# Kernel optimization log

Hardware: AMD Instinct MI355X
Metric: run time of the kernel (lower is better)

## Reference

```python
import jax, jax.numpy as jnp
import numpy as np

N = 50000      # nodes
K = 32         # fixed neighbor count per node
D_IN, D_HID, D_OUT = 512, 128, 64


def setup_inputs() -> dict:
    key = jax.random.key(0)
    k1, k2, k3, k4 = jax.random.split(key, 4)
    feat = jax.random.normal(k1, (N, D_IN), dtype=jnp.float32)
    W1 = jax.random.normal(k2, (D_IN, D_HID), dtype=jnp.float32) * (1.0 / np.sqrt(D_IN))
    b1 = jnp.zeros((D_HID,), dtype=jnp.float32)
    W2 = jax.random.normal(k3, (D_HID, D_OUT), dtype=jnp.float32) * (1.0 / np.sqrt(D_HID))
    b2 = jnp.zeros((D_OUT,), dtype=jnp.float32)
    neighbors = jax.random.randint(k4, (N, K), 0, N, dtype=jnp.int64)
    return {"feat": feat, "W1": W1, "b1": b1, "W2": W2, "b2": b2,
            "neighbors": neighbors}


def _median_conv(x, W, b, neighbors):
    # linear transform, then per-node median over neighbor messages
    h = x @ W + b                      # [N, D]
    nb = h[neighbors]                  # [N, K, D]  gather (irregular access)
    # torch.median returns the lower middle element for even K
    med = jnp.sort(nb, axis=1)[:, (K - 1) // 2]   # [N, D]
    return med


def reference(feat, W1, b1, W2, b2, neighbors):
    # MedianGCN forward (eval mode: dropout is identity), norm='none'
    h = jax.nn.relu(_median_conv(feat, W1, b1, neighbors))
    out = _median_conv(h, W2, b2, neighbors)
    return out
```

## Files before the change

### kernel.cpp

```cpp
#include <hip/hip_runtime.h>
#include <cstddef>

#define NN   50000
#define KNB  32

typedef _Float16 h2    __attribute__((ext_vector_type(2)));
typedef _Float16 half8 __attribute__((ext_vector_type(8)));
typedef float    f4    __attribute__((ext_vector_type(4)));
typedef float    f8    __attribute__((ext_vector_type(8)));

__global__ __launch_bounds__(256) void prep(const float* __restrict__ W1,
                                            const float* __restrict__ W2,
                                            _Float16* __restrict__ w1t,
                                            _Float16* __restrict__ w2t) {
  const int id = blockIdx.x * 256 + threadIdx.x;
  if (id < 128 * 512) {
    const int n = id >> 9, k = id & 511;
    w1t[id] = (_Float16)W1[k * 128 + n];
  } else {
    const int id2 = id - 128 * 512;
    if (id2 < 64 * 128) {
      const int n = id2 >> 7, k = id2 & 127;
      w2t[id2] = (_Float16)W2[k * 64 + n];
    }
  }
}

__global__ __launch_bounds__(256) void gemm1_mfma(
    const float* __restrict__ A, const _Float16* __restrict__ Bt,
    const float* __restrict__ bias, _Float16* __restrict__ C, int M) {
  constexpr int K = 512;
  const int wave = threadIdx.x >> 6;
  const int lane = threadIdx.x & 63;
  const int m0   = blockIdx.x * 64 + wave * 16;
  const int mr   = lane & 15;
  const int kg   = lane >> 4;

  int arow = m0 + mr;
  if (arow >= M) arow = M - 1;
  const float*    ap = A  + (size_t)arow * K + kg * 8;
  const _Float16* bp = Bt + (size_t)mr   * K + kg * 8;

  f4 acc[8] = {};

  #pragma unroll 2
  for (int k0 = 0; k0 < K; k0 += 32) {
    const f4 a0 = *(const f4*)ap;
    const f4 a1 = *(const f4*)(ap + 4);
    const f8 av = {a0[0], a0[1], a0[2], a0[3], a1[0], a1[1], a1[2], a1[3]};
    const half8 af = __builtin_convertvector(av, half8);
    #pragma unroll
    for (int nt = 0; nt < 8; ++nt) {
      const half8 bf = *(const half8*)(bp + (size_t)nt * 16 * K);
      acc[nt] = __builtin_amdgcn_mfma_f32_16x16x32_f16(af, bf, acc[nt], 0, 0, 0);
    }
    ap += 32;
    bp += 32;
  }

  #pragma unroll
  for (int nt = 0; nt < 8; ++nt) {
    const int col = nt * 16 + mr;
    const float bv = bias[col];
    #pragma unroll
    for (int r = 0; r < 4; ++r) {
      const int row = m0 + kg * 4 + r;
      if (row < M)
        C[(size_t)row * 128 + col] = (_Float16)(acc[nt][r] + bv);
    }
  }
}

__global__ __launch_bounds__(256) void gemm2_mfma(
    const _Float16* __restrict__ A, const _Float16* __restrict__ Bt,
    const float* __restrict__ bias, _Float16* __restrict__ C, int M) {
  constexpr int K = 128;
  const int wave = threadIdx.x >> 6;
  const int lane = threadIdx.x & 63;
  const int m0   = blockIdx.x * 64 + wave * 16;
  const int mr   = lane & 15;
  const int kg   = lane >> 4;

  int arow = m0 + mr;
  if (arow >= M) arow = M - 1;
  const _Float16* ap = A  + (size_t)arow * K + kg * 8;
  const _Float16* bp = Bt + (size_t)mr   * K + kg * 8;

  f4 acc[4] = {};

  #pragma unroll
  for (int k0 = 0; k0 < K; k0 += 32) {
    const half8 af = *(const half8*)ap;
    #pragma unroll
    for (int nt = 0; nt < 4; ++nt) {
      const half8 bf = *(const half8*)(bp + (size_t)nt * 16 * K);
      acc[nt] = __builtin_amdgcn_mfma_f32_16x16x32_f16(af, bf, acc[nt], 0, 0, 0);
    }
    ap += 32;
    bp += 32;
  }

  #pragma unroll
  for (int nt = 0; nt < 4; ++nt) {
    const int col = nt * 16 + mr;
    const float bv = bias[col];
    #pragma unroll
    for (int r = 0; r < 4; ++r) {
      const int row = m0 + kg * 4 + r;
      if (row < M)
        C[(size_t)row * 64 + col] = (_Float16)(acc[nt][r] + bv);
    }
  }
}

__device__ __forceinline__ void ceh(h2& a, h2& b) {
  h2 lo = __builtin_elementwise_min(a, b);
  h2 hi = __builtin_elementwise_max(a, b);
  a = lo;
  b = hi;
}

__device__ __forceinline__ void sort32h(h2 (&v)[32]) {
  #pragma unroll
  for (int p = 1; p < 32; p <<= 1) {
    #pragma unroll
    for (int k = p; k >= 1; k >>= 1) {
      #pragma unroll
      for (int j = k & (p - 1); j + k < 32; j += 2 * k) {
        #pragma unroll
        for (int i = 0; i < k; ++i) {
          if (i + j + k < 32) {
            if ((i + j) / (2 * p) == (i + j + k) / (2 * p)) {
              ceh(v[i + j], v[i + j + k]);
            }
          }
        }
      }
    }
  }
}

__global__ __launch_bounds__(256) void median_relu1(const h2* __restrict__ H,
                                                    const int* __restrict__ nb,
                                                    h2* __restrict__ O) {
  const int node = blockIdx.x * 4 + (threadIdx.x >> 6);
  const int lane = threadIdx.x & 63;
  const int* nrow = nb + (size_t)node * KNB;
  h2 v[32];
  #pragma unroll
  for (int j = 0; j < KNB; ++j) {
    const int idx = nrow[j];
    v[j] = H[(size_t)idx * 64 + lane];
  }
  sort32h(v);
  const h2 z = (h2)((_Float16)0);
  O[(size_t)node * 64 + lane] = __builtin_elementwise_max(v[15], z);
}

__global__ __launch_bounds__(256) void median2(const h2* __restrict__ H,
                                               const int* __restrict__ nb,
                                               float2* __restrict__ O) {
  const int node = blockIdx.x * 8 + (threadIdx.x >> 5);
  const int lane = threadIdx.x & 31;
  const int* nrow = nb + (size_t)node * KNB;
  h2 v[32];
  #pragma unroll
  for (int j = 0; j < KNB; ++j) {
    const int idx = nrow[j];
    v[j] = H[(size_t)idx * 32 + lane];
  }
  sort32h(v);
  float2 o;
  o.x = (float)v[15][0];
  o.y = (float)v[15][1];
  O[(size_t)node * 32 + lane] = o;
}

extern "C" void kernel_launch(void* const* d_in, const int* in_sizes, int n_in,
                              void* d_out, int out_size, void* d_ws, size_t ws_size,
                              hipStream_t stream) {
  const float* feat = (const float*)d_in[0];
  const float* W1   = (const float*)d_in[1];
  const float* b1   = (const float*)d_in[2];
  const float* W2   = (const float*)d_in[3];
  const float* b2   = (const float*)d_in[4];
  const int*   nb   = (const int*)d_in[5];
  float* out = (float*)d_out;

  _Float16* h1   = (_Float16*)d_ws;
  _Float16* med1 = h1 + (size_t)NN * 128;
  _Float16* w1t  = med1 + (size_t)NN * 128;
  _Float16* w2t  = w1t + 128 * 512;
  _Float16* h2b  = h1;

  prep<<<dim3(288), dim3(256), 0, stream>>>(W1, W2, w1t, w2t);
  gemm1_mfma<<<dim3((NN + 63) / 64), dim3(256), 0, stream>>>(feat, w1t, b1, h1, NN);
  median_relu1<<<dim3(NN / 4), dim3(256), 0, stream>>>(
      (const h2*)h1, nb, (h2*)med1);
  gemm2_mfma<<<dim3((NN + 63) / 64), dim3(256), 0, stream>>>(med1, w2t, b2, h2b, NN);
  median2<<<dim3(NN / 8), dim3(256), 0, stream>>>(
      (const h2*)h2b, nb, (float2*)out);
}
```

Measured before the change: 299.7 us.

## Stage GEMM A and B tiles through shared memory with cooperative loads

Both MFMA GEMM kernels now load each K-slice of A and the transposed weights cooperatively into padded LDS tiles. Waves then read their MFMA fragments from LDS instead of each wave fetching the whole B panel from global or L2 memory on its own. This cuts redundant global loads of the weights, which were read four times per block. In exchange it adds two block barriers per K step and no double buffering, so load latency is no longer overlapped with the MFMAs.

Measured after the change: 257.6 us. -14.0%, faster.

```diff
diff --git a/kernel.cpp b/kernel.cpp
--- a/kernel.cpp
+++ b/kernel.cpp
@@ -29,33 +29,47 @@
 __global__ __launch_bounds__(256) void gemm1_mfma(
     const float* __restrict__ A, const _Float16* __restrict__ Bt,
     const float* __restrict__ bias, _Float16* __restrict__ C, int M) {
-  constexpr int K = 512;
-  const int wave = threadIdx.x >> 6;
-  const int lane = threadIdx.x & 63;
-  const int m0   = blockIdx.x * 64 + wave * 16;
+  constexpr int K = 512, BM = 64, BK = 32;
+  __shared__ _Float16 Ah[BM][40];
+  __shared__ _Float16 Bh[128][40];
+  const int tid  = threadIdx.x;
+  const int wave = tid >> 6;
+  const int lane = tid & 63;
   const int mr   = lane & 15;
   const int kg   = lane >> 4;
-
-  int arow = m0 + mr;
-  if (arow >= M) arow = M - 1;
-  const float*    ap = A  + (size_t)arow * K + kg * 8;
-  const _Float16* bp = Bt + (size_t)mr   * K + kg * 8;
+  const int m0   = blockIdx.x * BM;
+
+  const int srow = tid >> 2;
+  const int sseg = (tid & 3) * 8;
+  int aRow = m0 + srow;
+  if (aRow >= M) aRow = M - 1;
+  const float*    ap  = A  + (size_t)aRow * K + sseg;
+  const _Float16* bp0 = Bt + (size_t)srow * K + sseg;
+  const _Float16* bp1 = Bt + (size_t)(64 + srow) * K + sseg;
 
   f4 acc[8] = {};
 
-  #pragma unroll 2
-  for (int k0 = 0; k0 < K; k0 += 32) {
-    const f4 a0 = *(const f4*)ap;
-    const f4 a1 = *(const f4*)(ap + 4);
-    const f8 av = {a0[0], a0[1], a0[2], a0[3], a1[0], a1[1], a1[2], a1[3]};
-    const half8 af = __builtin_convertvector(av, half8);
+  for (int k0 = 0; k0 < K; k0 += BK) {
+    const f4 t0 = *(const f4*)ap;
+    const f4 t1 = *(const f4*)(ap + 4);
+    const half8 blo = *(const half8*)bp0;
+    const half8 bhi = *(const half8*)bp1;
+    const f8 av = {t0[0], t0[1], t0[2], t0[3], t1[0], t1[1], t1[2], t1[3]};
+    *(half8*)&Ah[srow][sseg]      = __builtin_convertvector(av, half8);
+    *(half8*)&Bh[srow][sseg]      = blo;
+    *(half8*)&Bh[64 + srow][sseg] = bhi;
+    __syncthreads();
+
+    const half8 af = *(const half8*)&Ah[wave * 16 + mr][kg * 8];
     #pragma unroll
     for (int nt = 0; nt < 8; ++nt) {
-      const half8 bf = *(const half8*)(bp + (size_t)nt * 16 * K);
+      const half8 bf = *(const half8*)&Bh[nt * 16 + mr][kg * 8];
       acc[nt] = __builtin_amdgcn_mfma_f32_16x16x32_f16(af, bf, acc[nt], 0, 0, 0);
     }
-    ap += 32;
-    bp += 32;
+    __syncthreads();
+    ap += BK;
+    bp0 += BK;
+    bp1 += BK;
   }
 
   #pragma unroll
@@ -64,7 +78,7 @@
     const float bv = bias[col];
     #pragma unroll
     for (int r = 0; r < 4; ++r) {
-      const int row = m0 + kg * 4 + r;
+      const int row = m0 + wave * 16 + kg * 4 + r;
       if (row < M)
         C[(size_t)row * 128 + col] = (_Float16)(acc[nt][r] + bv);
     }
@@ -74,30 +88,40 @@
 __global__ __launch_bounds__(256) void gemm2_mfma(
     const _Float16* __restrict__ A, const _Float16* __restrict__ Bt,
     const float* __restrict__ bias, _Float16* __restrict__ C, int M) {
-  constexpr int K = 128;
-  const int wave = threadIdx.x >> 6;
-  const int lane = threadIdx.x & 63;
-  const int m0   = blockIdx.x * 64 + wave * 16;
+  constexpr int K = 128, BM = 64, BK = 32;
+  __shared__ _Float16 Ah[BM][40];
+  __shared__ _Float16 Bh[64][40];
+  const int tid  = threadIdx.x;
+  const int wave = tid >> 6;
+  const int lane = tid & 63;
   const int mr   = lane & 15;
   const int kg   = lane >> 4;
-
-  int arow = m0 + mr;
-  if (arow >= M) arow = M - 1;
-  const _Float16* ap = A  + (size_t)arow * K + kg * 8;
-  const _Float16* bp = Bt + (size_t)mr   * K + kg * 8;
+  const int m0   = blockIdx.x * BM;
+
+  const int srow = tid >> 2;
+  const int sseg = (tid & 3) * 8;
+  int aRow = m0 + srow;
+  if (aRow >= M) aRow = M - 1;
+  const _Float16* ap = A  + (size_t)aRow * K + sseg;
+  const _Float16* bp = Bt + (size_t)srow * K + sseg;
 
   f4 acc[4] = {};
 
   #pragma unroll
-  for (int k0 = 0; k0 < K; k0 += 32) {
-    const half8 af = *(const half8*)ap;
+  for (int k0 = 0; k0 < K; k0 += BK) {
+    *(half8*)&Ah[srow][sseg] = *(const half8*)ap;
+    *(half8*)&Bh[srow][sseg] = *(const half8*)bp;
+    __syncthreads();
+
+    const half8 af = *(const half8*)&Ah[wave * 16 + mr][kg * 8];
     #pragma unroll
     for (int nt = 0; nt < 4; ++nt) {
-      const half8 bf = *(const half8*)(bp + (size_t)nt * 16 * K);
+      const half8 bf = *(const half8*)&Bh[nt * 16 + mr][kg * 8];
       acc[nt] = __builtin_amdgcn_mfma_f32_16x16x32_f16(af, bf, acc[nt], 0, 0, 0);
     }
-    ap += 32;
-    bp += 32;
+    __syncthreads();
+    ap += BK;
+    bp += BK;
   }
 
   #pragma unroll
@@ -106,7 +130,7 @@
     const float bv = bias[col];
     #pragma unroll
     for (int r = 0; r < 4; ++r) {
-      const int row = m0 + kg * 4 + r;
+      const int row = m0 + wave * 16 + kg * 4 + r;
       if (row < M)
         C[(size_t)row * 64 + col] = (_Float16)(acc[nt][r] + bv);
     }
```
